# Kernel optimization log

Hardware: AMD Instinct MI355X
Metric: run time of the kernel (lower is better)

The kernel has to match this reference:

```python
import jax, jax.numpy as jnp
import numpy as np

H = 12          # num_attention_heads
D = 768         # hidden_size
R = 4           # channel_shrink_ratio
DH = D // H     # 64, attention_head_size
DL = D // R     # 192, layout hidden size
DHL = DH // R   # 16, layout head size
NEG = jnp.finfo(jnp.float32).min


def setup_inputs() -> dict:
    key = jax.random.key(0)
    ks = jax.random.split(key, 16)
    B, S = 8, 1024
    s = 0.02
    inp = {
        "hidden_states": jax.random.normal(ks[0], (B, S, D), jnp.float32),
        "layout_hidden_states": jax.random.normal(ks[1], (B, S, DL), jnp.float32),
        "attention_mask": jnp.ones((B, S), jnp.float32),
        "Wq": jax.random.normal(ks[2], (D, D), jnp.float32) * s,
        "bq": jnp.zeros((D,), jnp.float32),
        "Wk": jax.random.normal(ks[3], (D, D), jnp.float32) * s,
        "bk": jnp.zeros((D,), jnp.float32),
        "Wv": jax.random.normal(ks[4], (D, D), jnp.float32) * s,
        "bv": jnp.zeros((D,), jnp.float32),
        "Wlq": jax.random.normal(ks[5], (DL, DL), jnp.float32) * s,
        "blq": jnp.zeros((DL,), jnp.float32),
        "Wlk": jax.random.normal(ks[6], (DL, DL), jnp.float32) * s,
        "blk": jnp.zeros((DL,), jnp.float32),
        "Wlv": jax.random.normal(ks[7], (DL, DL), jnp.float32) * s,
        "blv": jnp.zeros((DL,), jnp.float32),
    }
    return inp


def _heads(x, hd):
    # [B,S,H*hd] -> [B,H,S,hd]
    B, S, _ = x.shape
    return x.reshape(B, S, H, hd).transpose(0, 2, 1, 3)


def reference(hidden_states, layout_hidden_states, attention_mask,
              Wq, bq, Wk, bk, Wv, bv, Wlq, blq, Wlk, blk, Wlv, blv):
    B, S, _ = hidden_states.shape
    q = _heads(hidden_states @ Wq.T + bq, DH)
    k = _heads(hidden_states @ Wk.T + bk, DH)
    v = _heads(hidden_states @ Wv.T + bv, DH)
    lq = _heads(layout_hidden_states @ Wlq.T + blq, DHL)
    lk = _heads(layout_hidden_states @ Wlk.T + blk, DHL)
    lv = _heads(layout_hidden_states @ Wlv.T + blv, DHL)

    scores = jnp.einsum('bhqd,bhkd->bhqk', q, k) / jnp.sqrt(jnp.float32(DH))
    lscores = jnp.einsum('bhqd,bhkd->bhqk', lq, lk) / jnp.sqrt(jnp.float32(DHL))
    fused = scores + lscores  # cross-added scores (same for both streams)

    bias = (1.0 - attention_mask)[:, None, None, :] * NEG  # [B,1,1,S]
    fused = fused + bias

    probs = jax.nn.softmax(fused, axis=-1)   # dropout disabled (p=0)

    ctx = jnp.einsum('bhqk,bhkd->bhqd', probs, v)
    ctx = ctx.transpose(0, 2, 1, 3).reshape(B, S, D)
    lctx = jnp.einsum('bhqk,bhkd->bhqd', probs, lv)
    lctx = lctx.transpose(0, 2, 1, 3).reshape(B, S, DL)
    return ctx, lctx, probs
```

## Files before the change

kernel.cpp:

```cpp
#include <hip/hip_runtime.h>

#define NH   12
#define SEQ  1024
#define NB   8
#define DCAT 96
#define DV   80

typedef __attribute__((ext_vector_type(8))) short  bf16x8;
typedef __attribute__((ext_vector_type(4))) float  f32x4;
typedef __attribute__((ext_vector_type(4))) unsigned short u16x4;

static __device__ __forceinline__ unsigned short f2bf(float x) {
    unsigned int u = __float_as_uint(x);
    u += 0x7fffu + ((u >> 16) & 1u);
    return (unsigned short)(u >> 16);
}
static __device__ __forceinline__ f32x4 fzero() {
    f32x4 z; z[0]=0.f; z[1]=0.f; z[2]=0.f; z[3]=0.f; return z;
}
static __device__ __forceinline__ unsigned int cvtpk(float lo, float hi) {
    unsigned int r;
    asm("v_cvt_pk_bf16_f32 %0, %1, %2" : "=v"(r) : "v"(lo), "v"(hi));
    return r;
}

#define GLDS16(gp, lp) __builtin_amdgcn_global_load_lds(                      \
    (const __attribute__((address_space(1))) void*)(gp),                      \
    (__attribute__((address_space(3))) void*)(lp), 16, 0, 0)

#define WAITV(nstr) asm volatile("s_waitcnt vmcnt(" nstr ")" ::: "memory")
#define SBARRIER() do {                                                       \
    __builtin_amdgcn_sched_barrier(0);                                        \
    asm volatile("" ::: "memory");                                            \
    __builtin_amdgcn_s_barrier();                                             \
    asm volatile("" ::: "memory");                                            \
    __builtin_amdgcn_sched_barrier(0);                                        \
} while (0)

__global__ __launch_bounds__(256) void cvt_all(
    const float* __restrict__ hs, const float* __restrict__ lhs,
    const float* __restrict__ Wq, const float* __restrict__ Wk, const float* __restrict__ Wv,
    const float* __restrict__ Wlq, const float* __restrict__ Wlk, const float* __restrict__ Wlv,
    unsigned short* __restrict__ hid16, unsigned short* __restrict__ lay16,
    unsigned short* __restrict__ wqkv16, unsigned short* __restrict__ wl16)
{
    int i = blockIdx.x * 256 + threadIdx.x;
    const float* src; unsigned short* dst; int off;
    if      (i < 1572864) { src = hs;  dst = hid16;           off = i; }
    else if (i < 1966080) { src = lhs; dst = lay16;           off = i - 1572864; }
    else if (i < 2113536) { src = Wq;  dst = wqkv16;          off = i - 1966080; }
    else if (i < 2260992) { src = Wk;  dst = wqkv16 + 589824; off = i - 2113536; }
    else if (i < 2408448) { src = Wv;  dst = wqkv16 + 1179648;off = i - 2260992; }
    else if (i < 2417664) { src = Wlq; dst = wl16;            off = i - 2408448; }
    else if (i < 2426880) { src = Wlk; dst = wl16 + 36864;    off = i - 2417664; }
    else if (i < 2436096) { src = Wlv; dst = wl16 + 73728;    off = i - 2426880; }
    else return;
    f32x4 v = ((const f32x4*)src)[off];
    u16x4 o;
    o[0] = f2bf(v[0]); o[1] = f2bf(v[1]); o[2] = f2bf(v[2]); o[3] = f2bf(v[3]);
    ((u16x4*)dst)[off] = o;
}

__global__ __launch_bounds__(256) void pad_fill(
    const float* __restrict__ mask,
    unsigned short* __restrict__ Qc, unsigned short* __restrict__ Kc)
{
    int i = blockIdx.x * 256 + threadIdx.x;
    if (i >= 98304) return;
    int bh = i >> 10, s = i & 1023;
    int b = bh / NH;
    float bias = (1.0f - mask[b * SEQ + s]) * -3.4028234663852886e38f;
    size_t idx = ((size_t)bh * SEQ + s) * DCAT + 80;
    Kc[idx] = f2bf(bias);
    Qc[idx] = 0x3F80;
}

__global__ __launch_bounds__(256) void proj_gemm(
    const unsigned short* __restrict__ Ahid,
    const unsigned short* __restrict__ Alay,
    const unsigned short* __restrict__ Bwqkv,
    const unsigned short* __restrict__ Bwl,
    const float* __restrict__ bq, const float* __restrict__ bk, const float* __restrict__ bv,
    const float* __restrict__ blq, const float* __restrict__ blk_, const float* __restrict__ blv,
    unsigned short* __restrict__ Qc, unsigned short* __restrict__ Kc, unsigned short* __restrict__ VT)
{
    __shared__ __align__(16) unsigned short As[4096];
    __shared__ __align__(16) unsigned short Bs[4096];
    const int tid = threadIdx.x, w = tid >> 6, lane = tid & 63;
    const int g = lane >> 4, c = lane & 15;

    const int variant = (blockIdx.y < 18) ? 0 : 1;
    const unsigned short* A  = variant ? Alay : Ahid;
    const unsigned short* Bw = variant ? Bwl  : Bwqkv;
    const float* b0 = variant ? blq  : bq;
    const float* b1 = variant ? blk_ : bk;
    const float* b2 = variant ? blv  : bv;
    const int K    = variant ? 192 : 768;
    const int Ntot = variant ? 576 : 2304;
    const int m0 = blockIdx.x * 128;
    const int n0 = (variant ? (blockIdx.y - 18) : blockIdx.y) * 128;

    const int wr = w >> 1, wc = w & 1;
    const int srow = lane >> 2, scol = (lane & 3) * 8;

    f32x4 acc[4][4];
    #pragma unroll
    for (int m = 0; m < 4; m++)
        #pragma unroll
        for (int n = 0; n < 4; n++) acc[m][n] = fzero();

    const int ch0 = w * 2, ch1 = w * 2 + 1;
    const size_t arow0 = (size_t)(m0 + ch0 * 16 + srow) * K + scol;
    const size_t arow1 = (size_t)(m0 + ch1 * 16 + srow) * K + scol;
    int bn0 = n0 + ch0 * 16 + srow; if (bn0 >= Ntot) bn0 = Ntot - 1;
    int bn1 = n0 + ch1 * 16 + srow; if (bn1 >= Ntot) bn1 = Ntot - 1;
    const size_t brow0 = (size_t)bn0 * K + scol;
    const size_t brow1 = (size_t)bn1 * K + scol;

    for (int k0 = 0; k0 < K; k0 += 32) {
        __syncthreads();
        GLDS16(A  + arow0 + k0, As + ch0 * 512);
        GLDS16(A  + arow1 + k0, As + ch1 * 512);
        GLDS16(Bw + brow0 + k0, Bs + ch0 * 512);
        GLDS16(Bw + brow1 + k0, Bs + ch1 * 512);
        __syncthreads();
        bf16x8 af[4], bfr[4];
        #pragma unroll
        for (int m = 0; m < 4; m++) af[m]  = *(const bf16x8*)&As[(wr*64 + m*16 + c)*32 + g*8];
        #pragma unroll
        for (int n = 0; n < 4; n++) bfr[n] = *(const bf16x8*)&Bs[(wc*64 + n*16 + c)*32 + g*8];
        #pragma unroll
        for (int m = 0; m < 4; m++)
            #pragma unroll
            for (int n = 0; n < 4; n++)
                acc[m][n] = __builtin_amdgcn_mfma_f32_16x16x32_bf16(af[m], bfr[n], acc[m][n], 0, 0, 0);
    }

    const int b_ = m0 >> 10;
    #pragma unroll
    for (int nf = 0; nf < 4; nf++) {
        int n = n0 + wc * 64 + nf * 16 + c;
        if (n >= Ntot) continue;
        int seg, nn;
        if (variant == 0) { seg = (n >= 1536) ? 2 : ((n >= 768) ? 1 : 0); nn = n - seg * 768; }
        else              { seg = (n >= 384)  ? 2 : ((n >= 192) ? 1 : 0); nn = n - seg * 192; }
        const float* bp = (seg == 0) ? b0 : ((seg == 1) ? b1 : b2);
        float bv = bp[nn];
        float scale = (seg == 0) ? (variant ? 0.25f : 0.125f) : 1.0f;
        int h, d;
        if (variant == 0) { h = nn >> 6; d = nn & 63; }
        else              { h = nn >> 4; d = 64 + (nn & 15); }
        #pragma unroll
        for (int m = 0; m < 4; m++) {
            int row = m0 + wr * 64 + m * 16 + 4 * g;
            int s = row & 1023;
            if (seg < 2) {
                unsigned short* dst = (seg == 0) ? Qc : Kc;
                size_t base = (size_t)(b_ * NH + h) * SEQ;
                #pragma unroll
                for (int r = 0; r < 4; r++) {
                    dst[(base + s + r) * DCAT + d] = f2bf((acc[m][nf][r] + bv) * scale);
                    if (variant == 1)
                        dst[(base + s + r) * DCAT + d + 16] = 0;
                }
            } else {
                u16x4 pk;
                #pragma unroll
                for (int r = 0; r < 4; r++) pk[r] = f2bf(acc[m][nf][r] + bv);
                int kb = s >> 5, ko = s & 31;
                *(u16x4*)&VT[(((size_t)(b_ * NH + h) * 32 + kb) * DV + d) * 32 + ko] = pk;
            }
        }
    }
}

__global__ __launch_bounds__(256, 3) void attn_kernel(
    const unsigned short* __restrict__ Qc,
    const unsigned short* __restrict__ Kc,
    const unsigned short* __restrict__ VT,
    float* __restrict__ ctx,
    float* __restrict__ lctx,
    float* __restrict__ probs)
{
    __shared__ __align__(16) unsigned short Ks[2 * 6144];
    __shared__ __align__(16) unsigned short pbuf[4][32][36];

    const int tid = threadIdx.x, w = tid >> 6, lane = tid & 63;
    const int g = lane >> 4, c = lane & 15;

    const int bid = blockIdx.x;
    const int xc = bid & 7, j = bid >> 3;
    const int bh = xc + 8 * (j >> 3);
    const int qt = j & 7;
    const int b = bh / NH, h = bh % NH;
    const int qrb = qt * 128 + w * 32;

    bf16x8 qa0, qa1, qa2, qb0, qb1, qb2;
    {
        const unsigned short* qr0 = &Qc[((size_t)bh * SEQ + qrb + c) * DCAT + g * 8];
        qa0 = *(const bf16x8*)(qr0);
        qa1 = *(const bf16x8*)(qr0 + 32);
        qa2 = *(const bf16x8*)(qr0 + 64);
        const unsigned short* qr1 = qr0 + 16 * DCAT;
        qb0 = *(const bf16x8*)(qr1);
        qb1 = *(const bf16x8*)(qr1 + 32);
        qb2 = *(const bf16x8*)(qr1 + 64);
    }
    const unsigned short* Kb = Kc + (size_t)bh * SEQ * DCAT;
    const unsigned short* Vb = VT + (size_t)bh * 32 * DV * 32;

    const int slot8 = (g ^ ((c >> 1) & 3)) * 8;

    const unsigned short* gsrc[3]; int gstep[3];
    #pragma unroll
    for (int r = 0; r < 3; r++) {
        const int m = tid + 256 * r;
        if (m < 384) {
            int p = m >> 7, row = (m >> 2) & 31, jj = m & 3;
            int jx = jj ^ ((row >> 1) & 3);
            gsrc[r]  = Kb + row * DCAT + p * 32 + jx * 8;
            gstep[r] = 32 * DCAT;
        } else if (m < 704) {
            int mv = m - 384;
            int df = mv >> 6, cc = (mv >> 2) & 15, jj = mv & 3;
            int jx = jj ^ ((cc >> 1) & 3);
            gsrc[r]  = Vb + (df * 16 + cc) * 32 + jx * 8;
            gstep[r] = DV * 32;
        } else {
            gsrc[r]  = Vb;
            gstep[r] = 0;
        }
    }
    const int dub = w * 512;

    f32x4 cacc0[5], cacc1[5];
    #pragma unroll
    for (int nf = 0; nf < 5; nf++) { cacc0[nf] = fzero(); cacc1[nf] = fzero(); }
    float sm0 = 0.f, sm1 = 0.f;

    #pragma unroll
    for (int r = 0; r < 3; r++)
        GLDS16(gsrc[r], Ks + r * 2048 + dub);
    __builtin_amdgcn_sched_barrier(0);

    for (int t = 0; t < 32; t++) {
        const int buf = t & 1;
        WAITV("0");
        SBARRIER();
        if (t < 31) {
            #pragma unroll
            for (int r = 0; r < 3; r++)
                GLDS16(gsrc[r] + (t + 1) * gstep[r], Ks + (buf ^ 1) * 6144 + r * 2048 + dub);
            __builtin_amdgcn_sched_barrier(0);
        }

        #pragma unroll
        for (int ktl = 0; ktl < 2; ktl++) {
            const int rb = buf * 6144 + (ktl * 16 + c) * 32 + slot8;
            bf16x8 k0 = *(const bf16x8*)&Ks[rb];
            bf16x8 k1 = *(const bf16x8*)&Ks[rb + 1024];
            bf16x8 k2 = *(const bf16x8*)&Ks[rb + 2048];
            f32x4 a0 = __builtin_amdgcn_mfma_f32_16x16x32_bf16(k0, qa0, fzero(), 0, 0, 0);
            f32x4 a1 = __builtin_amdgcn_mfma_f32_16x16x32_bf16(k1, qa1, fzero(), 0, 0, 0);
            f32x4 a2 = __builtin_amdgcn_mfma_f32_16x16x32_bf16(k2, qa2, fzero(), 0, 0, 0);
            f32x4 b0 = __builtin_amdgcn_mfma_f32_16x16x32_bf16(k0, qb0, fzero(), 0, 0, 0);
            f32x4 b1 = __builtin_amdgcn_mfma_f32_16x16x32_bf16(k1, qb1, fzero(), 0, 0, 0);
            f32x4 b2 = __builtin_amdgcn_mfma_f32_16x16x32_bf16(k2, qb2, fzero(), 0, 0, 0);
            f32x4 e0, e1;
            #pragma unroll
            for (int r = 0; r < 4; r++) {
                e0[r] = __expf(a0[r] + a1[r] + a2[r]);
                e1[r] = __expf(b0[r] + b1[r] + b2[r]);
                sm0 += e0[r];
                sm1 += e1[r];
            }
            uint2 hh0, hh1;
            hh0.x = cvtpk(e0[0], e0[1]); hh0.y = cvtpk(e0[2], e0[3]);
            hh1.x = cvtpk(e1[0], e1[1]); hh1.y = cvtpk(e1[2], e1[3]);
            *(uint2*)&pbuf[w][c][ktl * 16 + 4 * g]      = hh0;
            *(uint2*)&pbuf[w][16 + c][ktl * 16 + 4 * g] = hh1;
        }
        const int vb0 = buf * 6144 + 3072 + c * 32 + slot8;
        bf16x8 vf0 = *(const bf16x8*)&Ks[vb0];
        bf16x8 vf1 = *(const bf16x8*)&Ks[vb0 + 512];
        bf16x8 vf2 = *(const bf16x8*)&Ks[vb0 + 1024];
        bf16x8 vf3 = *(const bf16x8*)&Ks[vb0 + 1536];
        bf16x8 vf4 = *(const bf16x8*)&Ks[vb0 + 2048];
        bf16x8 pa0 = *(const bf16x8*)&pbuf[w][c][g * 8];
        bf16x8 pa1 = *(const bf16x8*)&pbuf[w][16 + c][g * 8];
        cacc0[0] = __builtin_amdgcn_mfma_f32_16x16x32_bf16(pa0, vf0, cacc0[0], 0, 0, 0);
        cacc1[0] = __builtin_amdgcn_mfma_f32_16x16x32_bf16(pa1, vf0, cacc1[0], 0, 0, 0);
        cacc0[1] = __builtin_amdgcn_mfma_f32_16x16x32_bf16(pa0, vf1, cacc0[1], 0, 0, 0);
        cacc1[1] = __builtin_amdgcn_mfma_f32_16x16x32_bf16(pa1, vf1, cacc1[1], 0, 0, 0);
        cacc0[2] = __builtin_amdgcn_mfma_f32_16x16x32_bf16(pa0, vf2, cacc0[2], 0, 0, 0);
        cacc1[2] = __builtin_amdgcn_mfma_f32_16x16x32_bf16(pa1, vf2, cacc1[2], 0, 0, 0);
        cacc0[3] = __builtin_amdgcn_mfma_f32_16x16x32_bf16(pa0, vf3, cacc0[3], 0, 0, 0);
        cacc1[3] = __builtin_amdgcn_mfma_f32_16x16x32_bf16(pa1, vf3, cacc1[3], 0, 0, 0);
        cacc0[4] = __builtin_amdgcn_mfma_f32_16x16x32_bf16(pa0, vf4, cacc0[4], 0, 0, 0);
        cacc1[4] = __builtin_amdgcn_mfma_f32_16x16x32_bf16(pa1, vf4, cacc1[4], 0, 0, 0);
    }

    sm0 += __shfl_xor(sm0, 16); sm0 += __shfl_xor(sm0, 32);
    sm1 += __shfl_xor(sm1, 16); sm1 += __shfl_xor(sm1, 32);
    const float rinv0 = 1.0f / fmaxf(sm0, 1e-38f);
    const float rinv1 = 1.0f / fmaxf(sm1, 1e-38f);

    float rl0[4], rl1[4];
    #pragma unroll
    for (int r = 0; r < 4; r++) {
        rl0[r] = __shfl(rinv0, 4 * g + r);
        rl1[r] = __shfl(rinv1, 4 * g + r);
    }

    #pragma unroll
    for (int nf = 0; nf < 4; nf++)
        #pragma unroll
        for (int r = 0; r < 4; r++) {
            int q0 = qrb + 4 * g + r;
            ctx[((size_t)(b * SEQ + q0)) * 768 + h * 64 + nf * 16 + c] = cacc0[nf][r] * rl0[r];
            ctx[((size_t)(b * SEQ + q0 + 16)) * 768 + h * 64 + nf * 16 + c] = cacc1[nf][r] * rl1[r];
        }
    #pragma unroll
    for (int r = 0; r < 4; r++) {
        int q0 = qrb + 4 * g + r;
        lctx[((size_t)(b * SEQ + q0)) * 192 + h * 16 + c] = cacc0[4][r] * rl0[r];
        lctx[((size_t)(b * SEQ + q0 + 16)) * 192 + h * 16 + c] = cacc1[4][r] * rl1[r];
    }

    const int srow   = lane >> 2;
    const int schunk = (lane & 3) ^ ((lane >> 3) & 3);
    const int ssrcA  = (w * 16 + srow) * DCAT + schunk * 8;
    unsigned short* sdstA = &Ks[w * 512];

    const size_t prow0 = ((size_t)bh * SEQ + qrb + c) * SEQ;
    const size_t prow1 = prow0 + 16 * SEQ;

    SBARRIER();
    #pragma unroll
    for (int p = 0; p < 3; p++) GLDS16(Kb + ssrcA + p * 32, sdstA + p * 2048);
    __builtin_amdgcn_sched_barrier(0);

    for (int t = 0; t < 16; t++) {
        const int buf = t & 1;
        if (t == 0) WAITV("0");
        else        WAITV("8");
        SBARRIER();
        if (t < 15) {
            const unsigned short* src = Kb + (t + 1) * 6144 + ssrcA;
            unsigned short* dst = sdstA + (buf ^ 1) * 6144;
            #pragma unroll
            for (int p = 0; p < 3; p++) GLDS16(src + p * 32, dst + p * 2048);
            __builtin_amdgcn_sched_barrier(0);
        }
        #pragma unroll
        for (int ktl = 0; ktl < 4; ktl++) {
            const int rb = buf * 6144 + (ktl * 16 + c) * 32 + slot8;
            bf16x8 k0 = *(const bf16x8*)&Ks[rb];
            bf16x8 k1 = *(const bf16x8*)&Ks[rb + 2048];
            bf16x8 k2 = *(const bf16x8*)&Ks[rb + 4096];
            f32x4 a0 = __builtin_amdgcn_mfma_f32_16x16x32_bf16(k0, qa0, fzero(), 0, 0, 0);
            f32x4 a1 = __builtin_amdgcn_mfma_f32_16x16x32_bf16(k1, qa1, fzero(), 0, 0, 0);
            f32x4 a2 = __builtin_amdgcn_mfma_f32_16x16x32_bf16(k2, qa2, fzero(), 0, 0, 0);
            f32x4 b0 = __builtin_amdgcn_mfma_f32_16x16x32_bf16(k0, qb0, fzero(), 0, 0, 0);
            f32x4 b1 = __builtin_amdgcn_mfma_f32_16x16x32_bf16(k1, qb1, fzero(), 0, 0, 0);
            f32x4 b2 = __builtin_amdgcn_mfma_f32_16x16x32_bf16(k2, qb2, fzero(), 0, 0, 0);
            f32x4 p0, p1;
            #pragma unroll
            for (int r = 0; r < 4; r++) {
                p0[r] = __expf(a0[r] + a1[r] + a2[r]) * rinv0;
                p1[r] = __expf(b0[r] + b1[r] + b2[r]) * rinv1;
            }
            *(f32x4*)&probs[prow0 + (t * 64 + ktl * 16) + 4 * g] = p0;
            *(f32x4*)&probs[prow1 + (t * 64 + ktl * 16) + 4 * g] = p1;
        }
    }
}

extern "C" void kernel_launch(void* const* d_in, const int* in_sizes, int n_in,
                              void* d_out, int out_size, void* d_ws, size_t ws_size,
                              hipStream_t stream)
{
    const float* hs   = (const float*)d_in[0];
    const float* lhs  = (const float*)d_in[1];
    const float* mask = (const float*)d_in[2];
    const float* Wq   = (const float*)d_in[3];
    const float* bq   = (const float*)d_in[4];
    const float* Wk   = (const float*)d_in[5];
    const float* bk   = (const float*)d_in[6];
    const float* Wv   = (const float*)d_in[7];
    const float* bv   = (const float*)d_in[8];
    const float* Wlq  = (const float*)d_in[9];
    const float* blq  = (const float*)d_in[10];
    const float* Wlk  = (const float*)d_in[11];
    const float* blk_ = (const float*)d_in[12];
    const float* Wlv  = (const float*)d_in[13];
    const float* blv  = (const float*)d_in[14];

    float* out   = (float*)d_out;
    float* ctx   = out;
    float* lctx  = out + (size_t)NB * SEQ * 768;
    float* probs = out + (size_t)NB * SEQ * 768 + (size_t)NB * SEQ * 192;

    char* ws = (char*)d_ws;
    unsigned short* Qc     = (unsigned short*)(ws);
    unsigned short* Kc     = (unsigned short*)(ws + 18874368);
    unsigned short* VT     = (unsigned short*)(ws + 37748736);
    unsigned short* hid16  = (unsigned short*)(ws + 53477376);
    unsigned short* lay16  = (unsigned short*)(ws + 66060288);
    unsigned short* wqkv16 = (unsigned short*)(ws + 69206016);
    unsigned short* wl16   = (unsigned short*)(ws + 72744960);

    cvt_all<<<dim3(9516), dim3(256), 0, stream>>>(hs, lhs, Wq, Wk, Wv, Wlq, Wlk, Wlv,
                                                  hid16, lay16, wqkv16, wl16);

    proj_gemm<<<dim3(64, 23), dim3(256), 0, stream>>>(hid16, lay16, wqkv16, wl16,
                                                      bq, bk, bv, blq, blk_, blv,
                                                      Qc, Kc, VT);

    pad_fill<<<dim3(384), dim3(256), 0, stream>>>(mask, Qc, Kc);

    attn_kernel<<<dim3(768), dim3(256), 0, stream>>>(Qc, Kc, VT, ctx, lctx, probs);
}
```

Before: 237.9 us.

## Split attention into context kernel and separate probs-writing kernel

The single attention kernel, which computed the context and then recomputed scores to write the normalized probabilities, is split into two launches. The first computes ctx/lctx and stores per-row inverse softmax sums to a workspace buffer. The second kernel recomputes QK^T over half the keys per block (twice as many blocks, higher occupancy bound) and writes the normalized probs using those stored sums. This aims to raise parallelism and occupancy in the store-bound probs phase, at the cost of an extra launch and a small round trip for the inverse sums.

```diff
diff --git a/kernel.cpp b/kernel.cpp
--- a/kernel.cpp
+++ b/kernel.cpp
@@ -174,13 +174,13 @@
     }
 }
 
-__global__ __launch_bounds__(256, 3) void attn_kernel(
+__global__ __launch_bounds__(256, 3) void attn_a(
     const unsigned short* __restrict__ Qc,
     const unsigned short* __restrict__ Kc,
     const unsigned short* __restrict__ VT,
     float* __restrict__ ctx,
     float* __restrict__ lctx,
-    float* __restrict__ probs)
+    float* __restrict__ rinvbuf)
 {
     __shared__ __align__(16) unsigned short Ks[2 * 6144];
     __shared__ __align__(16) unsigned short pbuf[4][32][36];
@@ -305,6 +305,11 @@
     const float rinv0 = 1.0f / fmaxf(sm0, 1e-38f);
     const float rinv1 = 1.0f / fmaxf(sm1, 1e-38f);
 
+    if (g == 0) {
+        rinvbuf[(size_t)bh * SEQ + qrb + c]      = rinv0;
+        rinvbuf[(size_t)bh * SEQ + qrb + 16 + c] = rinv1;
+    }
+
     float rl0[4], rl1[4];
     #pragma unroll
     for (int r = 0; r < 4; r++) {
@@ -326,26 +331,61 @@
         lctx[((size_t)(b * SEQ + q0)) * 192 + h * 16 + c] = cacc0[4][r] * rl0[r];
         lctx[((size_t)(b * SEQ + q0 + 16)) * 192 + h * 16 + c] = cacc1[4][r] * rl1[r];
     }
-
+}
+
+__global__ __launch_bounds__(256, 4) void attn_b(
+    const unsigned short* __restrict__ Qc,
+    const unsigned short* __restrict__ Kc,
+    const float* __restrict__ rinvbuf,
+    float* __restrict__ probs)
+{
+    __shared__ __align__(16) unsigned short Ks[2 * 6144];
+
+    const int tid = threadIdx.x, w = tid >> 6, lane = tid & 63;
+    const int g = lane >> 4, c = lane & 15;
+
+    const int bid = blockIdx.x;
+    const int xc = bid & 7, j = bid >> 3;
+    const int bh = xc + 8 * (j >> 4);
+    const int sub = j & 15;
+    const int qt = sub >> 1, kh = sub & 1;
+    const int qrb = qt * 128 + w * 32;
+
+    bf16x8 qa0, qa1, qa2, qb0, qb1, qb2;
+    {
+        const unsigned short* qr0 = &Qc[((size_t)bh * SEQ + qrb + c) * DCAT + g * 8];
+        qa0 = *(const bf16x8*)(qr0);
+        qa1 = *(const bf16x8*)(qr0 + 32);
+        qa2 = *(const bf16x8*)(qr0 + 64);
+        const unsigned short* qr1 = qr0 + 16 * DCAT;
+        qb0 = *(const bf16x8*)(qr1);
+        qb1 = *(const bf16x8*)(qr1 + 32);
+        qb2 = *(const bf16x8*)(qr1 + 64);
+    }
+    const unsigned short* Kb = Kc + (size_t)bh * SEQ * DCAT + (size_t)kh * 512 * DCAT;
+
+    const float rinv0 = rinvbuf[(size_t)bh * SEQ + qrb + c];
+    const float rinv1 = rinvbuf[(size_t)bh * SEQ + qrb + 16 + c];
+
+    const int slot8 = (g ^ ((c >> 1) & 3)) * 8;
     const int srow   = lane >> 2;
     const int schunk = (lane & 3) ^ ((lane >> 3) & 3);
     const int ssrcA  = (w * 16 + srow) * DCAT + schunk * 8;
     unsigned short* sdstA = &Ks[w * 512];
 
-    const size_t prow0 = ((size_t)bh * SEQ + qrb + c) * SEQ;
+    const size_t prow0 = ((size_t)bh * SEQ + qrb + c) * SEQ + kh * 512;
     const size_t prow1 = prow0 + 16 * SEQ;
 
-    SBARRIER();
     #pragma unroll
     for (int p = 0; p < 3; p++) GLDS16(Kb + ssrcA + p * 32, sdstA + p * 2048);
     __builtin_amdgcn_sched_barrier(0);
 
-    for (int t = 0; t < 16; t++) {
+    for (int t = 0; t < 8; t++) {
         const int buf = t & 1;
         if (t == 0) WAITV("0");
         else        WAITV("8");
         SBARRIER();
-        if (t < 15) {
+        if (t < 7) {
             const unsigned short* src = Kb + (t + 1) * 6144 + ssrcA;
             unsigned short* dst = sdstA + (buf ^ 1) * 6144;
             #pragma unroll
@@ -409,6 +449,7 @@
     unsigned short* lay16  = (unsigned short*)(ws + 66060288);
     unsigned short* wqkv16 = (unsigned short*)(ws + 69206016);
     unsigned short* wl16   = (unsigned short*)(ws + 72744960);
+    float*          rinvb  = (float*)(ws + 72966144);
 
     cvt_all<<<dim3(9516), dim3(256), 0, stream>>>(hs, lhs, Wq, Wk, Wv, Wlq, Wlk, Wlv,
                                                   hid16, lay16, wqkv16, wl16);
@@ -419,5 +460,6 @@
 
     pad_fill<<<dim3(384), dim3(256), 0, stream>>>(mask, Qc, Kc);
 
-    attn_kernel<<<dim3(768), dim3(256), 0, stream>>>(Qc, Kc, VT, ctx, lctx, probs);
-}
+    attn_a<<<dim3(768), dim3(256), 0, stream>>>(Qc, Kc, VT, ctx, lctx, rinvb);
+    attn_b<<<dim3(1536), dim3(256), 0, stream>>>(Qc, Kc, rinvb, probs);
+}
```

After: 229.8 us. -3.4%, faster.
